# Performance work log

Measured on AMD Instinct MI355X. Metric: run time of the kernel, lower is better.

Reference implementation:

```python
import jax, jax.numpy as jnp
import numpy as np

N_LAYERS = 12
N_HEADS = 12
D_MODEL = 768
VOCAB = 50257
T_WIN = 1024
B, T = 4, 1024
STD = 0.02


def setup_inputs() -> dict:
    key = jax.random.key(0)
    ks = jax.random.split(key, 8)
    inp = jax.random.randint(ks[0], (B, T), 0, VOCAB)
    target = jax.random.randint(ks[1], (B, T), 0, VOCAB)
    wte = jax.random.normal(ks[2], (VOCAB, D_MODEL), jnp.float32) * STD
    wpe = jax.random.normal(ks[3], (T_WIN, D_MODEL), jnp.float32) * STD
    attn_w = jax.random.normal(ks[4], (N_LAYERS, D_MODEL, 3 * D_MODEL), jnp.float32) * STD
    proj_w = jax.random.normal(ks[5], (N_LAYERS, D_MODEL, D_MODEL), jnp.float32) * STD
    fc_w = jax.random.normal(ks[6], (N_LAYERS, D_MODEL, 4 * D_MODEL), jnp.float32) * STD
    fc2_w = jax.random.normal(ks[7], (N_LAYERS, 4 * D_MODEL, D_MODEL), jnp.float32) * STD
    return {
        'inp': inp, 'target': target, 'wte': wte, 'wpe': wpe,
        'ln1_w': jnp.ones((N_LAYERS, D_MODEL), jnp.float32),
        'ln1_b': jnp.zeros((N_LAYERS, D_MODEL), jnp.float32),
        'attn_w': attn_w,
        'attn_b': jnp.zeros((N_LAYERS, 3 * D_MODEL), jnp.float32),
        'proj_w': proj_w,
        'proj_b': jnp.zeros((N_LAYERS, D_MODEL), jnp.float32),
        'ln2_w': jnp.ones((N_LAYERS, D_MODEL), jnp.float32),
        'ln2_b': jnp.zeros((N_LAYERS, D_MODEL), jnp.float32),
        'fc_w': fc_w,
        'fc_b': jnp.zeros((N_LAYERS, 4 * D_MODEL), jnp.float32),
        'fc2_w': fc2_w,
        'fc2_b': jnp.zeros((N_LAYERS, D_MODEL), jnp.float32),
        'lnf_w': jnp.ones((D_MODEL,), jnp.float32),
        'lnf_b': jnp.zeros((D_MODEL,), jnp.float32),
    }


def _layernorm(x, w, b, eps=1e-5):
    mu = jnp.mean(x, axis=-1, keepdims=True)
    var = jnp.var(x, axis=-1, keepdims=True)
    return (x - mu) * jax.lax.rsqrt(var + eps) * w + b


def _attention(x, w_qkv, b_qkv, w_proj, b_proj):
    b, t, c = x.shape
    hd = c // N_HEADS
    qkv = x @ w_qkv + b_qkv                      # [B,T,3C]
    q, k, v = jnp.split(qkv, 3, axis=-1)
    # [B,H,T,hd]
    q = q.reshape(b, t, N_HEADS, hd).transpose(0, 2, 1, 3)
    k = k.reshape(b, t, N_HEADS, hd).transpose(0, 2, 1, 3)
    v = v.reshape(b, t, N_HEADS, hd).transpose(0, 2, 1, 3)
    scores = jnp.einsum('bhqd,bhkd->bhqk', q, k) / jnp.sqrt(jnp.float32(hd))
    causal = jnp.tril(jnp.ones((t, t), bool))
    scores = jnp.where(causal[None, None], scores, -jnp.inf)
    w = jax.nn.softmax(scores, axis=-1)          # dropout p=0 (eval)
    ctx = jnp.einsum('bhqk,bhkd->bhqd', w, v)
    ctx = ctx.transpose(0, 2, 1, 3).reshape(b, t, c)
    return ctx @ w_proj + b_proj


def reference(inp, target, wte, wpe, ln1_w, ln1_b, attn_w, attn_b, proj_w, proj_b,
              ln2_w, ln2_b, fc_w, fc_b, fc2_w, fc2_b, lnf_w, lnf_b):
    b, t = inp.shape
    x = wte[inp] + wpe[:t][None]                 # [B,T,C]
    for i in range(N_LAYERS):
        x = x + _attention(_layernorm(x, ln1_w[i], ln1_b[i]),
                           attn_w[i], attn_b[i], proj_w[i], proj_b[i])
        h = _layernorm(x, ln2_w[i], ln2_b[i])
        h = jax.nn.gelu(h @ fc_w[i] + fc_b[i], approximate=True)
        x = x + (h @ fc2_w[i] + fc2_b[i])
    x = _layernorm(x, lnf_w, lnf_b)
    logits = x @ wte.T                            # tied lm_head, no bias
    logp = jax.nn.log_softmax(logits, axis=-1)
    nll = -jnp.take_along_axis(logp, target[..., None], axis=-1)[..., 0]
    loss = jnp.mean(nll)
    return logits, loss
```

## Files before the change

### kernel.cpp

```cpp
#include <hip/hip_runtime.h>
#include <hip/hip_bf16.h>
#include <cmath>

#define NLAYERS 12
#define NHEADS  12
#define DM      768
#define VOCAB   50257
#define TSEQ    1024
#define BT      4096
#define NCHUNK  786

typedef __attribute__((ext_vector_type(4))) float f32x4;
typedef __attribute__((ext_vector_type(8))) short bf16x8;
typedef __attribute__((ext_vector_type(4))) short s16x4;

typedef __hip_bfloat16 bf16;

#define MFMA16(a, b, c) __builtin_amdgcn_mfma_f32_16x16x32_bf16(a, b, c, 0, 0, 0)

__device__ __forceinline__ void gload16(const void* g, void* l) {
    __builtin_amdgcn_global_load_lds(
        (const __attribute__((address_space(1))) void*)g,
        (__attribute__((address_space(3))) void*)l, 16, 0, 0);
}

__device__ __forceinline__ void wg_barrier() {
    asm volatile("" ::: "memory");
    __builtin_amdgcn_s_barrier();
    asm volatile("" ::: "memory");
}

__device__ __forceinline__ float gelu_tanh(float v) {
    float u = 0.7978845608028654f * (v + 0.044715f * v * v * v);
    return 0.5f * v * (1.0f + tanhf(u));
}

__device__ __forceinline__ short f2bf(float f) {
    bf16 h = (bf16)f;
    return *reinterpret_cast<short*>(&h);
}

template<int CTRL>
__device__ __forceinline__ float dpp_mov(float x) {
    int i = __builtin_bit_cast(int, x);
    i = __builtin_amdgcn_mov_dpp(i, CTRL, 0xF, 0xF, false);
    return __builtin_bit_cast(float, i);
}
__device__ __forceinline__ float dpp_max16(float x) {
    x = fmaxf(x, dpp_mov<0xB1>(x));
    x = fmaxf(x, dpp_mov<0x4E>(x));
    x = fmaxf(x, dpp_mov<0x141>(x));
    x = fmaxf(x, dpp_mov<0x140>(x));
    return x;
}
__device__ __forceinline__ float dpp_sum16(float x) {
    x += dpp_mov<0xB1>(x);
    x += dpp_mov<0x4E>(x);
    x += dpp_mov<0x141>(x);
    x += dpp_mov<0x140>(x);
    return x;
}

struct ushort4s { short a, b, c, d; };

__global__ void transpose_bf16_kernel(const float* __restrict__ in, bf16* __restrict__ out,
                                      int K, int N) {
    __shared__ float tile[32][33];
    size_t lofs = (size_t)blockIdx.z * K * N;
    int k0 = blockIdx.y * 32, n0 = blockIdx.x * 32;
    int tx = threadIdx.x, ty = threadIdx.y;
#pragma unroll
    for (int i = 0; i < 32; i += 8)
        tile[ty + i][tx] = in[lofs + (size_t)(k0 + ty + i) * N + n0 + tx];
    __syncthreads();
#pragma unroll
    for (int i = 0; i < 32; i += 8)
        out[lofs + (size_t)(n0 + ty + i) * K + k0 + tx] = (bf16)tile[tx][ty + i];
}

__global__ void tobf16_kernel(const float* __restrict__ in, bf16* __restrict__ out, size_t n4) {
    size_t i = (size_t)blockIdx.x * 256 + threadIdx.x;
    if (i < n4) {
        float4 f = reinterpret_cast<const float4*>(in)[i];
        s16x4 o = {f2bf(f.x), f2bf(f.y), f2bf(f.z), f2bf(f.w)};
        *reinterpret_cast<s16x4*>(out + i * 4) = o;
    }
}

__global__ void embed_kernel(const int* __restrict__ inp, const float* __restrict__ wte,
                             const float* __restrict__ wpe, float* __restrict__ x) {
    int idx = blockIdx.x * 256 + threadIdx.x;
    int m = idx / (DM / 4), c4 = idx % (DM / 4);
    int tok = inp[m];
    int t = m & (TSEQ - 1);
    float4 a = reinterpret_cast<const float4*>(wte)[(size_t)tok * (DM / 4) + c4];
    float4 b = reinterpret_cast<const float4*>(wpe)[(size_t)t * (DM / 4) + c4];
    float4 o = {a.x + b.x, a.y + b.y, a.z + b.z, a.w + b.w};
    reinterpret_cast<float4*>(x)[idx] = o;
}

__global__ __launch_bounds__(256) void ln_kernel(const float* __restrict__ x,
                                                 const float* __restrict__ w,
                                                 const float* __restrict__ b,
                                                 bf16* __restrict__ y) {
    int tid = threadIdx.x, wv = tid >> 6, lane = tid & 63;
    int row = blockIdx.x * 4 + wv;
    const float4* xr = reinterpret_cast<const float4*>(x + (size_t)row * DM);
    float4 v[3];
    float s = 0.f, q = 0.f;
#pragma unroll
    for (int j = 0; j < 3; ++j) {
        v[j] = xr[lane + 64 * j];
        s += v[j].x + v[j].y + v[j].z + v[j].w;
        q += v[j].x * v[j].x + v[j].y * v[j].y + v[j].z * v[j].z + v[j].w * v[j].w;
    }
#pragma unroll
    for (int o = 1; o < 64; o <<= 1) { s += __shfl_xor(s, o); q += __shfl_xor(q, o); }
    float mu  = s * (1.0f / DM);
    float var = q * (1.0f / DM) - mu * mu;
    float inv = rsqrtf(var + 1e-5f);
#pragma unroll
    for (int j = 0; j < 3; ++j) {
        int c4 = lane + 64 * j;
        float4 wv4 = reinterpret_cast<const float4*>(w)[c4];
        float4 bv4 = reinterpret_cast<const float4*>(b)[c4];
        ushort4s o;
        o.a = f2bf((v[j].x - mu) * inv * wv4.x + bv4.x);
        o.b = f2bf((v[j].y - mu) * inv * wv4.y + bv4.y);
        o.c = f2bf((v[j].z - mu) * inv * wv4.z + bv4.z);
        o.d = f2bf((v[j].w - mu) * inv * wv4.w + bv4.w);
        *reinterpret_cast<ushort4s*>(y + (size_t)row * DM + c4 * 4) = o;
    }
}

#define GF_GELU    1
#define GF_OBF16   2
#define GF_CLAMP   4
#define GF_PARTIAL 8

template<int FLAGS, int TAG>
__global__ __launch_bounds__(256) void gemm_k(
    const bf16* __restrict__ A, const bf16* __restrict__ Bt,
    const float* __restrict__ bias, const float* __restrict__ resid,
    void* __restrict__ C, float2* __restrict__ partials,
    int M, int N, int K) {
    __shared__ short ldsA[3][128 * 32];
    __shared__ short ldsB[3][128 * 32];
    int tid = threadIdx.x;
    int lane = tid & 63, w = tid >> 6;
    int wm = w >> 1, wn = w & 1;
    int r = lane & 15, kq = lane >> 4;
    int bm = blockIdx.x * 128, bn = blockIdx.y * 128;

    f32x4 acc[4][4] = {};

    auto stage = [&](int buf, int kt) {
        int k0 = kt * 32;
#pragma unroll
        for (int i = 0; i < 2; ++i) {
            int chunk = i * 256 + tid;
            int row = chunk >> 2;
            int gs = (chunk & 3) ^ ((row >> 1) & 3);
            const bf16* ga = A + (size_t)(bm + row) * K + k0 + gs * 8;
            gload16(ga, &ldsA[buf][(i * 256 + w * 64) * 8]);
            int brow = bn + row;
            const bf16* gb = Bt + (size_t)brow * K + k0 + gs * 8;
            gload16(gb, &ldsB[buf][(i * 256 + w * 64) * 8]);
        }
    };
    auto compute = [&](int buf) {
        bf16x8 af[4], bfr[4];
#pragma unroll
        for (int m = 0; m < 4; ++m) {
            int row = wm * 64 + m * 16 + r;
            af[m] = *reinterpret_cast<bf16x8*>(&ldsA[buf][row * 32 + (kq ^ ((row >> 1) & 3)) * 8]);
        }
#pragma unroll
        for (int n = 0; n < 4; ++n) {
            int row = wn * 64 + n * 16 + r;
            bfr[n] = *reinterpret_cast<bf16x8*>(&ldsB[buf][row * 32 + (kq ^ ((row >> 1) & 3)) * 8]);
        }
        __builtin_amdgcn_s_setprio(1);
#pragma unroll
        for (int m = 0; m < 4; ++m)
#pragma unroll
            for (int n = 0; n < 4; ++n)
                acc[m][n] = MFMA16(af[m], bfr[n], acc[m][n]);
        __builtin_amdgcn_s_setprio(0);
    };

    const int NT = K / 32;
    stage(0, 0);
    stage(1, 1);
    for (int t = 0; t < NT; ++t) {
        if (t + 2 < NT) {
            stage((t + 2) % 3, t + 2);
            asm volatile("s_waitcnt vmcnt(8)" ::: "memory");
        } else if (t + 1 < NT) {
            asm volatile("s_waitcnt vmcnt(4)" ::: "memory");
        } else {
            asm volatile("s_waitcnt vmcnt(0)" ::: "memory");
        }
        wg_barrier();
        compute(t % 3);
        asm volatile("s_waitcnt lgkmcnt(0)" ::: "memory");
        wg_barrier();
    }

    int row0 = bm + wm * 64, col0 = bn + wn * 64;
#pragma unroll
    for (int m = 0; m < 4; ++m) {
#pragma unroll
        for (int n = 0; n < 4; ++n) {
            int col = col0 + n * 16 + r;
#pragma unroll
            for (int rr = 0; rr < 4; ++rr) {
                int row = row0 + m * 16 + kq * 4 + rr;
                float v = acc[m][n][rr];
                if (bias) v += bias[col];
                if (FLAGS & GF_GELU) v = gelu_tanh(v);
                if (resid) v += resid[(size_t)row * N + col];
                if (FLAGS & GF_OBF16) ((bf16*)C)[(size_t)row * N + col] = (bf16)v;
                else                  ((float*)C)[(size_t)row * N + col] = v;
            }
        }
    }
}

template<int FLAGS, int TAG>
__global__ __launch_bounds__(256) void gemm_k64(
    const bf16* __restrict__ A, const bf16* __restrict__ Bt,
    const float* __restrict__ bias, const float* __restrict__ resid,
    void* __restrict__ C, float2* __restrict__ partials,
    int M, int N, int K) {
    __shared__ short ldsA[3][64 * 32];
    __shared__ short ldsB[3][128 * 32];
    int tid = threadIdx.x;
    int lane = tid & 63, w = tid >> 6;
    int r = lane & 15, kq = lane >> 4;
    int bm = blockIdx.x * 64, bn = blockIdx.y * 128;

    f32x4 acc[4][2] = {};

    auto stage = [&](int buf, int kt) {
        int k0 = kt * 32;
        {
            int row = tid >> 2;
            int gs = (tid & 3) ^ ((row >> 1) & 3);
            gload16(A + (size_t)(bm + row) * K + k0 + gs * 8, &ldsA[buf][tid * 8]);
        }
#pragma unroll
        for (int i = 0; i < 2; ++i) {
            int chunk = i * 256 + tid;
            int row = chunk >> 2;
            int gs = (chunk & 3) ^ ((row >> 1) & 3);
            gload16(Bt + (size_t)(bn + row) * K + k0 + gs * 8, &ldsB[buf][chunk * 8]);
        }
    };
    auto compute = [&](int buf) {
        bf16x8 af[4], bfr[2];
#pragma unroll
        for (int m = 0; m < 4; ++m) {
            int row = m * 16 + r;
            af[m] = *reinterpret_cast<bf16x8*>(&ldsA[buf][row * 32 + (kq ^ ((row >> 1) & 3)) * 8]);
        }
#pragma unroll
        for (int n = 0; n < 2; ++n) {
            int row = w * 32 + n * 16 + r;
            bfr[n] = *reinterpret_cast<bf16x8*>(&ldsB[buf][row * 32 + (kq ^ ((row >> 1) & 3)) * 8]);
        }
        __builtin_amdgcn_s_setprio(1);
#pragma unroll
        for (int m = 0; m < 4; ++m)
#pragma unroll
            for (int n = 0; n < 2; ++n)
                acc[m][n] = MFMA16(af[m], bfr[n], acc[m][n]);
        __builtin_amdgcn_s_setprio(0);
    };

    const int NT = K / 32;
    stage(0, 0);
    stage(1, 1);
    for (int t = 0; t < NT; ++t) {
        if (t + 2 < NT) {
            stage((t + 2) % 3, t + 2);
            asm volatile("s_waitcnt vmcnt(6)" ::: "memory");
        } else if (t + 1 < NT) {
            asm volatile("s_waitcnt vmcnt(3)" ::: "memory");
        } else {
            asm volatile("s_waitcnt vmcnt(0)" ::: "memory");
        }
        wg_barrier();
        compute(t % 3);
        asm volatile("s_waitcnt lgkmcnt(0)" ::: "memory");
        wg_barrier();
    }

    int col0 = bn + w * 32;
#pragma unroll
    for (int m = 0; m < 4; ++m) {
#pragma unroll
        for (int n = 0; n < 2; ++n) {
            int col = col0 + n * 16 + r;
#pragma unroll
            for (int rr = 0; rr < 4; ++rr) {
                int row = bm + m * 16 + kq * 4 + rr;
                float v = acc[m][n][rr];
                if (bias) v += bias[col];
                if (FLAGS & GF_GELU) v = gelu_tanh(v);
                if (resid) v += resid[(size_t)row * N + col];
                if (FLAGS & GF_OBF16) ((bf16*)C)[(size_t)row * N + col] = (bf16)v;
                else                  ((float*)C)[(size_t)row * N + col] = v;
            }
        }
    }
}

template<int FLAGS, int TAG>
__global__ __launch_bounds__(512, 4) void gemm_wide(
    const bf16* __restrict__ A, const bf16* __restrict__ Bt,
    const float* __restrict__ bias, const float* __restrict__ resid,
    void* __restrict__ C, float2* __restrict__ partials,
    int M, int N, int K) {
    __shared__ short ldsA[3][128 * 32];
    __shared__ short ldsB[3][256 * 32];
    int tid = threadIdx.x;
    int lane = tid & 63, w = tid >> 6;
    int wm = w >> 2, wn = w & 3;
    int r = lane & 15, kq = lane >> 4;
    int bm = blockIdx.x * 128, bn = blockIdx.y * 256;

    f32x4 acc[4][4] = {};

    auto stage = [&](int buf, int kt) {
        int k0 = kt * 32;
        {
            int row = tid >> 2;
            int gs = (tid & 3) ^ ((row >> 1) & 3);
            gload16(A + (size_t)(bm + row) * K + k0 + gs * 8, &ldsA[buf][tid * 8]);
        }
#pragma unroll
        for (int i = 0; i < 2; ++i) {
            int chunk = i * 512 + tid;
            int row = chunk >> 2;
            int gs = (chunk & 3) ^ ((row >> 1) & 3);
            int grow = bn + row;
            if (FLAGS & GF_CLAMP) grow = min(grow, N - 1);
            gload16(Bt + (size_t)grow * K + k0 + gs * 8, &ldsB[buf][chunk * 8]);
        }
    };
    auto compute = [&](int buf) {
        bf16x8 af[4], bfr[4];
#pragma unroll
        for (int m = 0; m < 4; ++m) {
            int row = wm * 64 + m * 16 + r;
            af[m] = *reinterpret_cast<bf16x8*>(&ldsA[buf][row * 32 + (kq ^ ((row >> 1) & 3)) * 8]);
        }
#pragma unroll
        for (int n = 0; n < 4; ++n) {
            int row = wn * 64 + n * 16 + r;
            bfr[n] = *reinterpret_cast<bf16x8*>(&ldsB[buf][row * 32 + (kq ^ ((row >> 1) & 3)) * 8]);
        }
        __builtin_amdgcn_s_setprio(1);
#pragma unroll
        for (int m = 0; m < 4; ++m)
#pragma unroll
            for (int n = 0; n < 4; ++n)
                acc[m][n] = MFMA16(af[m], bfr[n], acc[m][n]);
        __builtin_amdgcn_s_setprio(0);
    };

    const int NT = K / 32;
    stage(0, 0);
    stage(1, 1);
    for (int t = 0; t < NT; ++t) {
        if (t + 2 < NT) {
            stage((t + 2) % 3, t + 2);
            asm volatile("s_waitcnt vmcnt(6)" ::: "memory");
        } else if (t + 1 < NT) {
            asm volatile("s_waitcnt vmcnt(3)" ::: "memory");
        } else {
            asm volatile("s_waitcnt vmcnt(0)" ::: "memory");
        }
        wg_barrier();
        compute(t % 3);
        asm volatile("s_waitcnt lgkmcnt(0)" ::: "memory");
        wg_barrier();
    }

    int row0 = bm + wm * 64, col0 = bn + wn * 64;
#pragma unroll
    for (int m = 0; m < 4; ++m) {
#pragma unroll
        for (int n = 0; n < 4; ++n) {
            int col = col0 + n * 16 + r;
            if (col < N) {
#pragma unroll
                for (int rr = 0; rr < 4; ++rr) {
                    int row = row0 + m * 16 + kq * 4 + rr;
                    float v = acc[m][n][rr];
                    if (bias) v += bias[col];
                    if (FLAGS & GF_GELU) v = gelu_tanh(v);
                    if (resid) v += resid[(size_t)row * N + col];
                    if (FLAGS & GF_OBF16) ((bf16*)C)[(size_t)row * N + col] = (bf16)v;
                    else                  ((float*)C)[(size_t)row * N + col] = v;
                }
            }
        }
    }

    if (FLAGS & GF_PARTIAL) {
        int chunk = (bn >> 6) + wn;
        if (chunk < NCHUNK) {
#pragma unroll
            for (int m = 0; m < 4; ++m) {
#pragma unroll
                for (int rr = 0; rr < 4; ++rr) {
                    float vals[4], mx = -INFINITY;
#pragma unroll
                    for (int n = 0; n < 4; ++n) {
                        int col = col0 + n * 16 + r;
                        float v = (col < N) ? acc[m][n][rr] : -INFINITY;
                        vals[n] = v;
                        mx = fmaxf(mx, v);
                    }
                    mx = dpp_max16(mx);
                    float sum = 0.f;
#pragma unroll
                    for (int n = 0; n < 4; ++n)
                        if (vals[n] > -INFINITY) sum += __expf(vals[n] - mx);
                    sum = dpp_sum16(sum);
                    if (r == 0) {
                        int row = row0 + m * 16 + kq * 4 + rr;
                        partials[(size_t)row * NCHUNK + chunk] = make_float2(mx, sum);
                    }
                }
            }
        }
    }
}

__global__ __launch_bounds__(512, 4) void flash_attn_kernel(const bf16* __restrict__ qkv,
                                                            bf16* __restrict__ ctx) {
    __shared__ short Ks[128 * 64];
    __shared__ short Vt[64 * 128];
    __shared__ short Ps[8][16][132];

    int tid = threadIdx.x, lane = tid & 63, w = tid >> 6;
    int r = lane & 15, kq = lane >> 4;
    int qt = (int)gridDim.x - 1 - (int)blockIdx.x;
    int q0 = qt * 128;
    int bh = blockIdx.y;
    int b = bh / NHEADS, h = bh % NHEADS;
    const int RS = 3 * DM;

    const bf16* qbase = qkv + (size_t)(b * TSEQ + q0 + w * 16 + r) * RS + h * 64;
    bf16x8 qf[2];
    qf[0] = *reinterpret_cast<const bf16x8*>(qbase + kq * 8);
    qf[1] = *reinterpret_cast<const bf16x8*>(qbase + 32 + kq * 8);

    f32x4 of[4] = {};
    float mrow[4] = {-INFINITY, -INFINITY, -INFINITY, -INFINITY};
    float lrow[4] = {};

    int stid = tid & 255;
    int kvq = stid >> 3;
    int d0 = (stid & 7) * 8;
    bool isK = tid < 256;
    const bf16* sb0 = qkv + (size_t)(b * TSEQ) * RS + (isK ? DM : 2 * DM) + h * 64;
    bf16x8 r0, r1, r2, r3;

    auto loadKV = [&](int t) {
        const bf16* p = sb0 + (size_t)(t * 128 + kvq * 4) * RS + d0;
        r0 = *reinterpret_cast<const bf16x8*>(p);
        r1 = *reinterpret_cast<const bf16x8*>(p + RS);
        r2 = *reinterpret_cast<const bf16x8*>(p + 2 * RS);
        r3 = *reinterpret_cast<const bf16x8*>(p + 3 * RS);
    };
    auto writeKV = [&]() {
        if (isK) {
            bf16x8 rs[4] = {r0, r1, r2, r3};
#pragma unroll
            for (int j = 0; j < 4; ++j) {
                int kv = kvq * 4 + j;
                int pg = (stid & 7) ^ (kv & 7);
                *reinterpret_cast<bf16x8*>(&Ks[kv * 64 + pg * 8]) = rs[j];
            }
        } else {
            int lg = kvq >> 1, half = kvq & 1;
#pragma unroll
            for (int jj = 0; jj < 8; ++jj) {
                int d = d0 + jj;
                int phys = lg ^ (d & 7);
                s16x4 pk = {r0[jj], r1[jj], r2[jj], r3[jj]};
                *reinterpret_cast<s16x4*>(&Vt[d * 128 + phys * 8 + half * 4]) = pk;
            }
        }
    };

    int ntiles = qt + 1;
    loadKV(0);
    for (int t = 0; t < ntiles; ++t) {
        __syncthreads();
        writeKV();
        __syncthreads();
        if (t + 1 < ntiles) loadKV(t + 1);

        int kv0 = t * 128;
        f32x4 sf[8];
#pragma unroll
        for (int n = 0; n < 8; ++n) sf[n] = (f32x4){0.f, 0.f, 0.f, 0.f};
        __builtin_amdgcn_s_setprio(1);
#pragma unroll
        for (int n = 0; n < 8; ++n) {
            int row = n * 16 + r;
#pragma unroll
            for (int kt = 0; kt < 2; ++kt) {
                int gran = (kt * 4 + kq) ^ (row & 7);
                bf16x8 kf = *reinterpret_cast<bf16x8*>(&Ks[row * 64 + gran * 8]);
                sf[n] = MFMA16(qf[kt], kf, sf[n]);
            }
        }
        __builtin_amdgcn_s_setprio(0);

        bool diag = (kv0 + 128 > q0);
        float alpha[4];
#pragma unroll
        for (int rr = 0; rr < 4; ++rr) {
            int qrow = q0 + w * 16 + kq * 4 + rr;
            float vals[8];
            float mx = mrow[rr];
#pragma unroll
            for (int n = 0; n < 8; ++n) {
                float v = sf[n][rr] * 0.125f;
                if (diag && (kv0 + n * 16 + r) > qrow) v = -INFINITY;
                vals[n] = v;
                mx = fmaxf(mx, v);
            }
            mx = dpp_max16(mx);
            float al = __expf(mrow[rr] - mx);
            float sum = 0.f;
#pragma unroll
            for (int n = 0; n < 8; ++n) {
                float p = __expf(vals[n] - mx);
                vals[n] = p;
                sum += p;
            }
            sum = dpp_sum16(sum);
            mrow[rr] = mx;
            lrow[rr] = lrow[rr] * al + sum;
            alpha[rr] = al;
#pragma unroll
            for (int n = 0; n < 8; ++n) Ps[w][kq * 4 + rr][n * 16 + r] = f2bf(vals[n]);
        }
#pragma unroll
        for (int n = 0; n < 4; ++n)
#pragma unroll
            for (int rr = 0; rr < 4; ++rr) of[n][rr] *= alpha[rr];

        __builtin_amdgcn_s_setprio(1);
#pragma unroll
        for (int kt = 0; kt < 4; ++kt) {
            bf16x8 pa = *reinterpret_cast<bf16x8*>(&Ps[w][r][kt * 32 + kq * 8]);
#pragma unroll
            for (int n = 0; n < 4; ++n) {
                int row = n * 16 + r;
                int gran = (kt * 4 + kq) ^ (row & 7);
                bf16x8 vf = *reinterpret_cast<bf16x8*>(&Vt[row * 128 + gran * 8]);
                of[n] = MFMA16(pa, vf, of[n]);
            }
        }
        __builtin_amdgcn_s_setprio(0);
    }

#pragma unroll
    for (int rr = 0; rr < 4; ++rr) {
        float inv = 1.0f / lrow[rr];
        int qrow = q0 + w * 16 + kq * 4 + rr;
        bf16* cb = ctx + (size_t)(b * TSEQ + qrow) * DM + h * 64;
#pragma unroll
        for (int n = 0; n < 4; ++n) cb[n * 16 + r] = (bf16)(of[n][rr] * inv);
    }
}

__global__ __launch_bounds__(256) void loss_reduce_kernel(const float2* __restrict__ partials,
                                                          const float* __restrict__ logits,
                                                          const int* __restrict__ target,
                                                          float* __restrict__ nll) {
    int row = blockIdx.x, tid = threadIdx.x;
    const float2* pr = partials + (size_t)row * NCHUNK;
    float m = -INFINITY, s = 0.f;
    for (int c = tid; c < NCHUNK; c += 256) {
        float2 p = pr[c];
        if (p.x > m) { s = s * __expf(m - p.x) + p.y; m = p.x; }
        else         { s += p.y * __expf(p.x - m); }
    }
    __shared__ float sm[256], ssum[256];
    sm[tid] = m; ssum[tid] = s; __syncthreads();
    for (int o = 128; o; o >>= 1) {
        if (tid < o) {
            float m2 = sm[tid + o], s2 = ssum[tid + o];
            float mm = fmaxf(sm[tid], m2);
            ssum[tid] = ssum[tid] * __expf(sm[tid] - mm) + s2 * __expf(m2 - mm);
            sm[tid] = mm;
        }
        __syncthreads();
    }
    if (tid == 0) {
        float lse = sm[0] + logf(ssum[0]);
        nll[row] = lse - logits[(size_t)row * VOCAB + target[row]];
    }
}

__global__ void loss2_kernel(const float* __restrict__ nll, float* __restrict__ loss) {
    int tid = threadIdx.x;
    float s = 0.f;
    for (int i = tid; i < BT; i += 1024) s += nll[i];
    __shared__ float r[1024];
    r[tid] = s; __syncthreads();
    for (int o = 512; o; o >>= 1) { if (tid < o) r[tid] += r[tid + o]; __syncthreads(); }
    if (tid == 0) *loss = r[0] * (1.0f / BT);
}

extern "C" void kernel_launch(void* const* d_in, const int* in_sizes, int n_in,
                              void* d_out, int out_size, void* d_ws, size_t ws_size,
                              hipStream_t stream) {
    const int*   inp    = (const int*)  d_in[0];
    const int*   target = (const int*)  d_in[1];
    const float* wte    = (const float*)d_in[2];
    const float* wpe    = (const float*)d_in[3];
    const float* ln1_w  = (const float*)d_in[4];
    const float* ln1_b  = (const float*)d_in[5];
    const float* attn_w = (const float*)d_in[6];
    const float* attn_b = (const float*)d_in[7];
    const float* proj_w = (const float*)d_in[8];
    const float* proj_b = (const float*)d_in[9];
    const float* ln2_w  = (const float*)d_in[10];
    const float* ln2_b  = (const float*)d_in[11];
    const float* fc_w   = (const float*)d_in[12];
    const float* fc_b   = (const float*)d_in[13];
    const float* fc2_w  = (const float*)d_in[14];
    const float* fc2_b  = (const float*)d_in[15];
    const float* lnf_w  = (const float*)d_in[16];
    const float* lnf_b  = (const float*)d_in[17];
    float* out = (float*)d_out;

    char* p = (char*)d_ws;
    auto alloc = [&](size_t bytes) { char* q = p; p += (bytes + 255) & ~(size_t)255; return q; };
    float* x     = (float*)alloc((size_t)BT * DM * 4);
    float* nll   = (float*)alloc((size_t)BT * 4);
    bf16*  qkvb  = (bf16*) alloc((size_t)BT * 3 * DM * 2);
    bf16*  tmpb  = (bf16*) alloc((size_t)BT * DM * 2);
    bf16*  ctxb  = (bf16*) alloc((size_t)BT * DM * 2);
    bf16*  hb    = (bf16*) alloc((size_t)BT * 4 * DM * 2);
    bf16*  wteb  = (bf16*) alloc((size_t)VOCAB * DM * 2);
    bf16*  wqkvT = (bf16*) alloc((size_t)NLAYERS * 3 * DM * DM * 2);
    bf16*  wprojT= (bf16*) alloc((size_t)NLAYERS * DM * DM * 2);
    bf16*  wfcT  = (bf16*) alloc((size_t)NLAYERS * 4 * DM * DM * 2);
    bf16*  wfc2T = (bf16*) alloc((size_t)NLAYERS * 4 * DM * DM * 2);
    float2* partials = (float2*)ctxb;

    dim3 tb(32, 8);
    transpose_bf16_kernel<<<dim3(3 * DM / 32, DM / 32, NLAYERS), tb, 0, stream>>>(attn_w, wqkvT, DM, 3 * DM);
    transpose_bf16_kernel<<<dim3(DM / 32, DM / 32, NLAYERS), tb, 0, stream>>>(proj_w, wprojT, DM, DM);
    transpose_bf16_kernel<<<dim3(4 * DM / 32, DM / 32, NLAYERS), tb, 0, stream>>>(fc_w, wfcT, DM, 4 * DM);
    transpose_bf16_kernel<<<dim3(DM / 32, 4 * DM / 32, NLAYERS), tb, 0, stream>>>(fc2_w, wfc2T, 4 * DM, DM);
    {
        size_t n4 = (size_t)VOCAB * DM / 4;
        tobf16_kernel<<<(unsigned)((n4 + 255) / 256), 256, 0, stream>>>(wte, wteb, n4);
    }

    embed_kernel<<<BT * DM / 4 / 256, 256, 0, stream>>>(inp, wte, wpe, x);

    for (int i = 0; i < NLAYERS; ++i) {
        ln_kernel<<<BT / 4, 256, 0, stream>>>(x, ln1_w + i * DM, ln1_b + i * DM, tmpb);
        gemm_k<GF_OBF16, 0><<<dim3(BT / 128, 3 * DM / 128), 256, 0, stream>>>(
            tmpb, wqkvT + (size_t)i * 3 * DM * DM, attn_b + i * 3 * DM, nullptr,
            qkvb, nullptr, BT, 3 * DM, DM);
        flash_attn_kernel<<<dim3(TSEQ / 128, 4 * NHEADS), 512, 0, stream>>>(qkvb, ctxb);
        gemm_k64<0, 1><<<dim3(BT / 64, DM / 128), 256, 0, stream>>>(
            ctxb, wprojT + (size_t)i * DM * DM, proj_b + i * DM, x,
            x, nullptr, BT, DM, DM);
        ln_kernel<<<BT / 4, 256, 0, stream>>>(x, ln2_w + i * DM, ln2_b + i * DM, tmpb);
        gemm_k<GF_GELU | GF_OBF16, 2><<<dim3(BT / 128, 4 * DM / 128), 256, 0, stream>>>(
            tmpb, wfcT + (size_t)i * 4 * DM * DM, fc_b + i * 4 * DM, nullptr,
            hb, nullptr, BT, 4 * DM, DM);
        gemm_k64<0, 3><<<dim3(BT / 64, DM / 128), 256, 0, stream>>>(
            hb, wfc2T + (size_t)i * 4 * DM * DM, fc2_b + i * DM, x,
            x, nullptr, BT, DM, 4 * DM);
    }

    ln_kernel<<<BT / 4, 256, 0, stream>>>(x, lnf_w, lnf_b, tmpb);
    gemm_wide<GF_CLAMP | GF_PARTIAL, 4><<<dim3(BT / 128, (VOCAB + 255) / 256), 512, 0, stream>>>(
        tmpb, wteb, nullptr, nullptr, out, partials, BT, VOCAB, DM);
    loss_reduce_kernel<<<BT, 256, 0, stream>>>(partials, out, target, nll);
    loss2_kernel<<<1, 1024, 0, stream>>>(nll, out + (size_t)out_size - 1);
}
```

Baseline: 3.619 ms.

## Deepen GEMM K-tile to 64 with double buffering and wider LDS swizzle

```diff
diff --git a/kernel.cpp b/kernel.cpp
--- a/kernel.cpp
+++ b/kernel.cpp
@@ -144,8 +144,8 @@
     const float* __restrict__ bias, const float* __restrict__ resid,
     void* __restrict__ C, float2* __restrict__ partials,
     int M, int N, int K) {
-    __shared__ short ldsA[3][128 * 32];
-    __shared__ short ldsB[3][128 * 32];
+    __shared__ short ldsA[2][128 * 64];
+    __shared__ short ldsB[2][128 * 64];
     int tid = threadIdx.x;
     int lane = tid & 63, w = tid >> 6;
     int wm = w >> 1, wn = w & 1;
@@ -155,56 +155,63 @@
     f32x4 acc[4][4] = {};
 
     auto stage = [&](int buf, int kt) {
-        int k0 = kt * 32;
-#pragma unroll
-        for (int i = 0; i < 2; ++i) {
+        int k0 = kt * 64;
+#pragma unroll
+        for (int i = 0; i < 4; ++i) {
             int chunk = i * 256 + tid;
-            int row = chunk >> 2;
-            int gs = (chunk & 3) ^ ((row >> 1) & 3);
-            const bf16* ga = A + (size_t)(bm + row) * K + k0 + gs * 8;
-            gload16(ga, &ldsA[buf][(i * 256 + w * 64) * 8]);
-            int brow = bn + row;
-            const bf16* gb = Bt + (size_t)brow * K + k0 + gs * 8;
-            gload16(gb, &ldsB[buf][(i * 256 + w * 64) * 8]);
+            int row = chunk >> 3;
+            int gs = (chunk & 7) ^ (row & 7);
+            gload16(A + (size_t)(bm + row) * K + k0 + gs * 8, &ldsA[buf][chunk * 8]);
+        }
+#pragma unroll
+        for (int i = 0; i < 4; ++i) {
+            int chunk = i * 256 + tid;
+            int row = chunk >> 3;
+            int gs = (chunk & 7) ^ (row & 7);
+            gload16(Bt + (size_t)(bn + row) * K + k0 + gs * 8, &ldsB[buf][chunk * 8]);
         }
     };
     auto compute = [&](int buf) {
-        bf16x8 af[4], bfr[4];
-#pragma unroll
-        for (int m = 0; m < 4; ++m) {
-            int row = wm * 64 + m * 16 + r;
-            af[m] = *reinterpret_cast<bf16x8*>(&ldsA[buf][row * 32 + (kq ^ ((row >> 1) & 3)) * 8]);
-        }
-#pragma unroll
-        for (int n = 0; n < 4; ++n) {
-            int row = wn * 64 + n * 16 + r;
-            bfr[n] = *reinterpret_cast<bf16x8*>(&ldsB[buf][row * 32 + (kq ^ ((row >> 1) & 3)) * 8]);
-        }
         __builtin_amdgcn_s_setprio(1);
 #pragma unroll
-        for (int m = 0; m < 4; ++m)
-#pragma unroll
-            for (int n = 0; n < 4; ++n)
-                acc[m][n] = MFMA16(af[m], bfr[n], acc[m][n]);
+        for (int kk = 0; kk < 2; ++kk) {
+            bf16x8 af[4], bfr[4];
+#pragma unroll
+            for (int m = 0; m < 4; ++m) {
+                int row = wm * 64 + m * 16 + r;
+                af[m] = *reinterpret_cast<bf16x8*>(
+                    &ldsA[buf][row * 64 + ((kk * 4 + kq) ^ (row & 7)) * 8]);
+            }
+#pragma unroll
+            for (int n = 0; n < 4; ++n) {
+                int row = wn * 64 + n * 16 + r;
+                bfr[n] = *reinterpret_cast<bf16x8*>(
+                    &ldsB[buf][row * 64 + ((kk * 4 + kq) ^ (row & 7)) * 8]);
+            }
+#pragma unroll
+            for (int m = 0; m < 4; ++m)
+#pragma unroll
+                for (int n = 0; n < 4; ++n)
+                    acc[m][n] = MFMA16(af[m], bfr[n], acc[m][n]);
+        }
         __builtin_amdgcn_s_setprio(0);
     };
 
-    const int NT = K / 32;
+    const int NT = K / 64;
     stage(0, 0);
-    stage(1, 1);
+    int buf = 0;
     for (int t = 0; t < NT; ++t) {
-        if (t + 2 < NT) {
-            stage((t + 2) % 3, t + 2);
+        if (t + 1 < NT) {
+            stage(buf ^ 1, t + 1);
             asm volatile("s_waitcnt vmcnt(8)" ::: "memory");
-        } else if (t + 1 < NT) {
-            asm volatile("s_waitcnt vmcnt(4)" ::: "memory");
         } else {
             asm volatile("s_waitcnt vmcnt(0)" ::: "memory");
         }
         wg_barrier();
-        compute(t % 3);
+        compute(buf);
         asm volatile("s_waitcnt lgkmcnt(0)" ::: "memory");
         wg_barrier();
+        buf ^= 1;
     }
 
     int row0 = bm + wm * 64, col0 = bn + wn * 64;
@@ -233,8 +240,8 @@
     const float* __restrict__ bias, const float* __restrict__ resid,
     void* __restrict__ C, float2* __restrict__ partials,
     int M, int N, int K) {
-    __shared__ short ldsA[3][64 * 32];
-    __shared__ short ldsB[3][128 * 32];
+    __shared__ short ldsA[2][64 * 64];
+    __shared__ short ldsB[2][128 * 64];
     int tid = threadIdx.x;
     int lane = tid & 63, w = tid >> 6;
     int r = lane & 15, kq = lane >> 4;
@@ -243,57 +250,63 @@
     f32x4 acc[4][2] = {};
 
     auto stage = [&](int buf, int kt) {
-        int k0 = kt * 32;
-        {
-            int row = tid >> 2;
-            int gs = (tid & 3) ^ ((row >> 1) & 3);
-            gload16(A + (size_t)(bm + row) * K + k0 + gs * 8, &ldsA[buf][tid * 8]);
-        }
+        int k0 = kt * 64;
 #pragma unroll
         for (int i = 0; i < 2; ++i) {
             int chunk = i * 256 + tid;
-            int row = chunk >> 2;
-            int gs = (chunk & 3) ^ ((row >> 1) & 3);
+            int row = chunk >> 3;
+            int gs = (chunk & 7) ^ (row & 7);
+            gload16(A + (size_t)(bm + row) * K + k0 + gs * 8, &ldsA[buf][chunk * 8]);
+        }
+#pragma unroll
+        for (int i = 0; i < 4; ++i) {
+            int chunk = i * 256 + tid;
+            int row = chunk >> 3;
+            int gs = (chunk & 7) ^ (row & 7);
             gload16(Bt + (size_t)(bn + row) * K + k0 + gs * 8, &ldsB[buf][chunk * 8]);
         }
     };
     auto compute = [&](int buf) {
-        bf16x8 af[4], bfr[2];
-#pragma unroll
-        for (int m = 0; m < 4; ++m) {
-            int row = m * 16 + r;
-            af[m] = *reinterpret_cast<bf16x8*>(&ldsA[buf][row * 32 + (kq ^ ((row >> 1) & 3)) * 8]);
-        }
-#pragma unroll
-        for (int n = 0; n < 2; ++n) {
-            int row = w * 32 + n * 16 + r;
-            bfr[n] = *reinterpret_cast<bf16x8*>(&ldsB[buf][row * 32 + (kq ^ ((row >> 1) & 3)) * 8]);
-        }
         __builtin_amdgcn_s_setprio(1);
 #pragma unroll
-        for (int m = 0; m < 4; ++m)
-#pragma unroll
-            for (int n = 0; n < 2; ++n)
-                acc[m][n] = MFMA16(af[m], bfr[n], acc[m][n]);
+        for (int kk = 0; kk < 2; ++kk) {
+            bf16x8 af[4], bfr[2];
+#pragma unroll
+            for (int m = 0; m < 4; ++m) {
+                int row = m * 16 + r;
+                af[m] = *reinterpret_cast<bf16x8*>(
+                    &ldsA[buf][row * 64 + ((kk * 4 + kq) ^ (row & 7)) * 8]);
+            }
+#pragma unroll
+            for (int n = 0; n < 2; ++n) {
+                int row = w * 32 + n * 16 + r;
+                bfr[n] = *reinterpret_cast<bf16x8*>(
+                    &ldsB[buf][row * 64 + ((kk * 4 + kq) ^ (row & 7)) * 8]);
+            }
+#pragma unroll
+            for (int m = 0; m < 4; ++m)
+#pragma unroll
+                for (int n = 0; n < 2; ++n)
+                    acc[m][n] = MFMA16(af[m], bfr[n], acc[m][n]);
+        }
         __builtin_amdgcn_s_setprio(0);
     };
 
-    const int NT = K / 32;
+    const int NT = K / 64;
     stage(0, 0);
-    stage(1, 1);
+    int buf = 0;
     for (int t = 0; t < NT; ++t) {
-        if (t + 2 < NT) {
-            stage((t + 2) % 3, t + 2);
+        if (t + 1 < NT) {
+            stage(buf ^ 1, t + 1);
             asm volatile("s_waitcnt vmcnt(6)" ::: "memory");
-        } else if (t + 1 < NT) {
-            asm volatile("s_waitcnt vmcnt(3)" ::: "memory");
         } else {
             asm volatile("s_waitcnt vmcnt(0)" ::: "memory");
         }
         wg_barrier();
-        compute(t % 3);
+        compute(buf);
         asm volatile("s_waitcnt lgkmcnt(0)" ::: "memory");
         wg_barrier();
+        buf ^= 1;
     }
 
     int col0 = bn + w * 32;
@@ -403,7 +416,7 @@
                     if (FLAGS & GF_GELU) v = gelu_tanh(v);
                     if (resid) v += resid[(size_t)row * N + col];
                     if (FLAGS & GF_OBF16) ((bf16*)C)[(size_t)row * N + col] = (bf16)v;
-                    else                  ((float*)C)[(size_t)row * N + col] = v;
+                    else __builtin_nontemporal_store(v, &((float*)C)[(size_t)row * N + col]);
                 }
             }
         }
```

New measurement: 4.354 ms. +20.3%, slower.
